# Kernel optimization log

Measured on AMD Instinct MI355X. Metric: run time of the kernel, lower is better.

The kernel has to match this reference:

```python
import jax, jax.numpy as jnp
import numpy as np

H = W = 224
WS = 7          # window size
SS = 3          # shift size
NH = 12         # num heads
N = WS * WS     # tokens per window (49)


def _attn_mask():
    # shift-window attention mask, computed from static ints (numpy)
    img = np.zeros((H, W), np.float32)
    cnt = 0
    for h0, h1 in [(0, H - WS), (H - WS, H - SS), (H - SS, H)]:
        for w0, w1 in [(0, W - WS), (W - WS, W - SS), (W - SS, W)]:
            img[h0:h1, w0:w1] = cnt
            cnt += 1
    mw = img.reshape(H // WS, WS, W // WS, WS).transpose(0, 2, 1, 3).reshape(-1, N)
    diff = mw[:, None, :] - mw[:, :, None]          # (nW, N, N)
    m = np.where(diff != 0, -100.0, 0.0).astype(np.float32)
    return m[:, None, :, :]                         # (nW, 1, N, N)


def _rel_pos_index():
    coords = np.stack(np.meshgrid(np.arange(WS), np.arange(WS), indexing='ij'))
    cf = coords.reshape(2, -1)
    rc = (cf[:, :, None] - cf[:, None, :]).transpose(1, 2, 0)  # (N, N, 2)
    rc[..., 0] += WS - 1
    rc[..., 1] += WS - 1
    rc[..., 0] *= 2 * WS - 1
    return rc.sum(-1).reshape(-1)                    # (N*N,)


_MASK = _attn_mask()
_RPI = _rel_pos_index()


def _ln(x, w, b, eps=1e-5):
    mu = jnp.mean(x, -1, keepdims=True)
    var = jnp.mean((x - mu) ** 2, -1, keepdims=True)
    return (x - mu) / jnp.sqrt(var + eps) * w + b


def setup_inputs() -> dict:
    key = jax.random.key(0)
    ks = jax.random.split(key, 12)
    C, CM = 384, 1536
    s = 0.02
    return {
        'x': jax.random.normal(ks[0], (1, H * W, C), jnp.float32),
        'rpb_table': jax.random.normal(ks[1], (169, NH), jnp.float32) * s,
        'qkv_w': jax.random.normal(ks[2], (3 * C, C), jnp.float32) * s,
        'qkv_b': jax.random.normal(ks[3], (3 * C,), jnp.float32) * s,
        'proj_w': jax.random.normal(ks[4], (C, C), jnp.float32) * s,
        'proj_b': jax.random.normal(ks[5], (C,), jnp.float32) * s,
        'fc1_w': jax.random.normal(ks[6], (CM, C), jnp.float32) * s,
        'fc1_b': jax.random.normal(ks[7], (CM,), jnp.float32) * s,
        'fc2_w': jax.random.normal(ks[8], (C, CM), jnp.float32) * s,
        'fc2_b': jax.random.normal(ks[9], (C,), jnp.float32) * s,
        'norm1_w': jnp.ones((C,), jnp.float32),
        'norm1_b': jnp.zeros((C,), jnp.float32),
        'norm2_w': jnp.ones((C,), jnp.float32),
        'norm2_b': jnp.zeros((C,), jnp.float32),
    }


def reference(x, rpb_table, qkv_w, qkv_b, proj_w, proj_b, fc1_w, fc1_b,
              fc2_w, fc2_b, norm1_w, norm1_b, norm2_w, norm2_b):
    B, L, C = x.shape
    hd = C // NH
    scale = hd ** -0.5
    mask = jnp.asarray(_MASK)                        # (nW, 1, N, N)
    rpi = jnp.asarray(_RPI)

    shortcut = x
    h = _ln(x, norm1_w, norm1_b).reshape(B, H, W, C)
    h = jnp.roll(h, (-SS, -SS), axis=(1, 2))
    # window partition -> (B*nW, N, C)
    win = h.reshape(B, H // WS, WS, W // WS, WS, C).transpose(0, 1, 3, 2, 4, 5)
    win = win.reshape(-1, N, C)

    qkv = (win @ qkv_w.T + qkv_b).reshape(-1, N, 3, NH, hd).transpose(2, 0, 3, 1, 4)
    q, k, v = qkv[0] * scale, qkv[1], qkv[2]         # (nW, NH, N, hd)
    attn = jnp.einsum('whnd,whmd->whnm', q, k)
    bias = rpb_table[rpi].reshape(N, N, NH).transpose(2, 0, 1)[None]  # (1, NH, N, N)
    attn = jax.nn.softmax(attn + bias + mask, axis=-1)
    out = jnp.einsum('whnm,whmd->whnd', attn, v).transpose(0, 2, 1, 3).reshape(-1, N, C)
    out = out @ proj_w.T + proj_b

    # window reverse + unshift
    h = out.reshape(B, H // WS, W // WS, WS, WS, C).transpose(0, 1, 3, 2, 4, 5)
    h = h.reshape(B, H, W, C)
    h = jnp.roll(h, (SS, SS), axis=(1, 2)).reshape(B, L, C)

    x = shortcut + h
    y = _ln(x, norm2_w, norm2_b)
    y = jax.nn.gelu(y @ fc1_w.T + fc1_b, approximate=False)  # torch nn.GELU = erf
    y = y @ fc2_w.T + fc2_b
    return x + y
```

## Files before the change

kernel.cpp:

```cpp
#include <hip/hip_runtime.h>
#include <cstdint>
#include <cstddef>

#define AS1 __attribute__((address_space(1)))
#define AS3 __attribute__((address_space(3)))

typedef __attribute__((ext_vector_type(8))) short bf16x8;
typedef __attribute__((ext_vector_type(4))) short short4v;
typedef __attribute__((ext_vector_type(8))) unsigned short u16x8;
typedef __attribute__((ext_vector_type(4))) float f32x4;
typedef __attribute__((ext_vector_type(4))) unsigned short u16x4;

__device__ __forceinline__ float b2f(uint16_t u){ return __uint_as_float(((uint32_t)u) << 16); }
__device__ __forceinline__ uint16_t f2b(float f){
    uint32_t u = __float_as_uint(f);
    return (uint16_t)((u + 0x7fffu + ((u >> 16) & 1u)) >> 16);
}

__device__ __forceinline__ int pixof(int r){
    int w  = r / 49, t = r - w * 49;
    int wh = w >> 5, ww = w & 31;
    int th = t / 7,  tw = t - th * 7;
    int hp = wh * 7 + th + 3; if (hp >= 224) hp -= 224;
    int wp = ww * 7 + tw + 3; if (wp >= 224) wp -= 224;
    return hp * 224 + wp;
}

__global__ void f2b_kernel(const float* __restrict__ in, uint16_t* __restrict__ out, int n){
    int i = blockIdx.x * 256 + threadIdx.x;
    if (i < n) out[i] = f2b(in[i]);
}

template<int PERM>
__global__ __launch_bounds__(256) void ln_kernel(const float* __restrict__ in,
        const float* __restrict__ g, const float* __restrict__ b, uint16_t* __restrict__ out){
    int wave = threadIdx.x >> 6, lane = threadIdx.x & 63;
    int r = blockIdx.x * 4 + wave;
    int p = PERM ? pixof(r) : r;
    const float* row = in + (size_t)p * 384;
    float a[6];
    #pragma unroll
    for (int i = 0; i < 6; ++i) a[i] = row[lane * 6 + i];
    float s = 0.f, q = 0.f;
    #pragma unroll
    for (int i = 0; i < 6; ++i){ s += a[i]; q += a[i] * a[i]; }
    #pragma unroll
    for (int o = 32; o; o >>= 1){ s += __shfl_xor(s, o); q += __shfl_xor(q, o); }
    float mu   = s * (1.f / 384.f);
    float var  = q * (1.f / 384.f) - mu * mu;
    float rstd = rsqrtf(var + 1e-5f);
    uint16_t* orow = out + (size_t)r * 384;
    #pragma unroll
    for (int i = 0; i < 6; ++i){
        int c = lane * 6 + i;
        orow[c] = f2b((a[i] - mu) * rstd * g[c] + b[c]);
    }
}

template<int EPI>
__global__ __launch_bounds__(256, 2) void gemm_bt(
        const uint16_t* __restrict__ A, const uint16_t* __restrict__ B,
        const float* __restrict__ bias, void* __restrict__ outp,
        const float* __restrict__ xres, int N, int K, int row0)
{
    __shared__ alignas(16) uint16_t lA[128 * 32];
    __shared__ alignas(16) uint16_t lB[128 * 32];
    int tid  = threadIdx.x;
    int lane = tid & 63, wave = tid >> 6;

    int nwg = gridDim.x, bid = blockIdx.x;
    int q8 = nwg >> 3, r8 = nwg & 7;
    int xcd = bid & 7, idx = bid >> 3;
    int wg = (xcd < r8 ? xcd * (q8 + 1) : r8 * (q8 + 1) + (xcd - r8) * q8) + idx;

    int nt = N >> 7;
    int bm = wg / nt, bn = wg - bm * nt;
    int wr = wave >> 1, wc = wave & 1;
    int fr = lane & 15, kc = lane >> 4;

    const uint16_t* Ab = A + (size_t)(bm * 128) * K;
    const uint16_t* Bb = B + (size_t)(bn * 128) * K;
    int row_s = tid >> 2, slot = tid & 3;
    int kchunk = slot ^ (row_s & 3);
    const uint16_t* gA = Ab + (size_t)row_s * K + kchunk * 8;
    const uint16_t* gB = Bb + (size_t)row_s * K + kchunk * 8;
    AS3 char* sA = (AS3 char*)lA;
    AS3 char* sB = (AS3 char*)lB;

    f32x4 acc[4][4] = {};
    for (int k0 = 0; k0 < K; k0 += 32){
        __builtin_amdgcn_global_load_lds((const AS1 void*)(gA + k0),
                                         (AS3 void*)(sA + wave * 1024), 16, 0, 0);
        __builtin_amdgcn_global_load_lds((const AS1 void*)(gA + k0 + (size_t)64 * K),
                                         (AS3 void*)(sA + wave * 1024 + 4096), 16, 0, 0);
        __builtin_amdgcn_global_load_lds((const AS1 void*)(gB + k0),
                                         (AS3 void*)(sB + wave * 1024), 16, 0, 0);
        __builtin_amdgcn_global_load_lds((const AS1 void*)(gB + k0 + (size_t)64 * K),
                                         (AS3 void*)(sB + wave * 1024 + 4096), 16, 0, 0);
        __syncthreads();
        bf16x8 af[4], bv[4];
        #pragma unroll
        for (int m = 0; m < 4; ++m){
            int row = wr * 64 + m * 16 + fr;
            int byt = (row * 64 + kc * 16) ^ ((row & 3) << 4);
            af[m] = *(const bf16x8*)((const char*)lA + byt);
        }
        #pragma unroll
        for (int n = 0; n < 4; ++n){
            int row = wc * 64 + n * 16 + fr;
            int byt = (row * 64 + kc * 16) ^ ((row & 3) << 4);
            bv[n] = *(const bf16x8*)((const char*)lB + byt);
        }
        #pragma unroll
        for (int m = 0; m < 4; ++m)
            #pragma unroll
            for (int n = 0; n < 4; ++n)
                acc[m][n] = __builtin_amdgcn_mfma_f32_16x16x32_bf16(af[m], bv[n], acc[m][n], 0, 0, 0);
        __syncthreads();
    }

    int colb = bn * 128 + wc * 64 + fr;
    int rowb = bm * 128 + wr * 64 + ((lane >> 4) << 2);
    float bvv[4];
    #pragma unroll
    for (int n = 0; n < 4; ++n) bvv[n] = bias[colb + n * 16];

    if constexpr (EPI == 0 || EPI == 1 || EPI == 5){
        uint16_t* out = (uint16_t*)outp;
        #pragma unroll
        for (int m = 0; m < 4; ++m)
            #pragma unroll
            for (int rg = 0; rg < 4; ++rg){
                size_t rr = (size_t)(rowb + m * 16 + rg) * N;
                #pragma unroll
                for (int n = 0; n < 4; ++n){
                    int col = colb + n * 16;
                    float v = acc[m][n][rg] + bvv[n];
                    if constexpr (EPI == 1) v = 0.5f * v * (1.f + erff(v * 0.7071067811865475f));
                    if constexpr (EPI == 5){ if (col < 384) v *= 0.1767766952966369f; }
                    out[rr + col] = f2b(v);
                }
            }
    } else if constexpr (EPI == 2){
        float* out = (float*)outp;
        #pragma unroll
        for (int m = 0; m < 4; ++m)
            #pragma unroll
            for (int rg = 0; rg < 4; ++rg){
                int r = row0 + rowb + m * 16 + rg;
                size_t pb = (size_t)pixof(r) * 384;
                #pragma unroll
                for (int n = 0; n < 4; ++n){
                    int c = colb + n * 16;
                    out[pb + c] = xres[pb + c] + acc[m][n][rg] + bvv[n];
                }
            }
    } else {
        float* out = (float*)outp;
        #pragma unroll
        for (int m = 0; m < 4; ++m)
            #pragma unroll
            for (int rg = 0; rg < 4; ++rg){
                size_t rb2 = (size_t)(rowb + m * 16 + rg) * 384;
                #pragma unroll
                for (int n = 0; n < 4; ++n){
                    int c = colb + n * 16;
                    out[rb2 + c] = out[rb2 + c] + acc[m][n][rg] + bvv[n];
                }
            }
    }
}

__global__ __launch_bounds__(256) void attn_mfma(const uint16_t* __restrict__ qkv,
        const float* __restrict__ rpb, uint16_t* __restrict__ out)
{
    __shared__ float bl[4][208];
    __shared__ uint16_t vtl[4][32][68];
    int wv = threadIdx.x >> 6, lane = threadIdx.x & 63;
    int p = blockIdx.x * 4 + wv;
    int w = p / 12, h = p - w * 12;
    for (int i = lane; i < 169; i += 64) bl[wv][i] = rpb[i * 12 + h];

    const uint16_t* base = qkv + (size_t)(w * 49) * 1152 + h * 32;

    #pragma unroll
    for (int it = 0; it < 4; ++it){
        int u = it * 64 + lane;
        int t = u >> 2, dq = u & 3;
        if (t < 49){
            u16x8 v8 = *(const u16x8*)(base + (size_t)t * 1152 + 768 + dq * 8);
            #pragma unroll
            for (int j = 0; j < 8; ++j) vtl[wv][dq * 8 + j][t] = v8[j];
        } else {
            #pragma unroll
            for (int j = 0; j < 8; ++j) vtl[wv][dq * 8 + j][t] = 0;
        }
    }

    int c = lane & 15, g = lane >> 4;

    bf16x8 qf[4], kf[4];
    #pragma unroll
    for (int nt = 0; nt < 4; ++nt) qf[nt] = *(const bf16x8*)(base + (size_t)(16 * nt + c) * 1152 + g * 8);
    #pragma unroll
    for (int mt = 0; mt < 4; ++mt) kf[mt] = *(const bf16x8*)(base + (size_t)(16 * mt + c) * 1152 + 384 + g * 8);

    f32x4 zero = {0.f, 0.f, 0.f, 0.f};
    f32x4 sv[4][4];
    #pragma unroll
    for (int mt = 0; mt < 4; ++mt)
        #pragma unroll
        for (int nt = 0; nt < 4; ++nt)
            sv[mt][nt] = __builtin_amdgcn_mfma_f32_16x16x32_bf16(kf[mt], qf[nt], zero, 0, 0, 0);

    int wh = w >> 5, ww = w & 31;
    bool edge = (wh == 31) || (ww == 31);
    int ihq[4], iwq[4], regi[4];
    #pragma unroll
    for (int nt = 0; nt < 4; ++nt){
        int q = 16 * nt + c;
        int ih = (q * 37) >> 8; int iw = q - 7 * ih;
        ihq[nt] = ih; iwq[nt] = iw;
        int hi = wh * 7 + ih, wi = ww * 7 + iw;
        regi[nt] = (hi < 217 ? 0 : (hi < 221 ? 1 : 2)) * 3 + (wi < 217 ? 0 : (wi < 221 ? 1 : 2));
    }
    #pragma unroll
    for (int mt = 0; mt < 4; ++mt){
        #pragma unroll
        for (int r = 0; r < 4; ++r){
            int kt = 16 * mt + 4 * g + r;
            int jh = (kt * 37) >> 8; int jw = kt - 7 * jh;
            int hj = wh * 7 + jh, wj = ww * 7 + jw;
            int regj = (hj < 217 ? 0 : (hj < 221 ? 1 : 2)) * 3 + (wj < 217 ? 0 : (wj < 221 ? 1 : 2));
            #pragma unroll
            for (int nt = 0; nt < 4; ++nt){
                float b = bl[wv][(ihq[nt] - jh + 6) * 13 + (iwq[nt] - jw + 6)];
                float add = b + ((edge && regj != regi[nt]) ? -100.f : 0.f);
                float val = sv[mt][nt][r] + add;
                sv[mt][nt][r] = (kt < 49) ? val : -1e9f;
            }
        }
    }

    float inv[4];
    #pragma unroll
    for (int nt = 0; nt < 4; ++nt){
        float mx = -1e30f;
        #pragma unroll
        for (int mt = 0; mt < 4; ++mt)
            #pragma unroll
            for (int r = 0; r < 4; ++r) mx = fmaxf(mx, sv[mt][nt][r]);
        mx = fmaxf(mx, __shfl_xor(mx, 16));
        mx = fmaxf(mx, __shfl_xor(mx, 32));
        float sum = 0.f;
        #pragma unroll
        for (int mt = 0; mt < 4; ++mt)
            #pragma unroll
            for (int r = 0; r < 4; ++r){
                float e = __expf(sv[mt][nt][r] - mx);
                sv[mt][nt][r] = e; sum += e;
            }
        sum += __shfl_xor(sum, 16);
        sum += __shfl_xor(sum, 32);
        inv[nt] = 1.f / sum;
    }

    unsigned pk[4][4][2];
    #pragma unroll
    for (int nt = 0; nt < 4; ++nt)
        #pragma unroll
        for (int mt = 0; mt < 4; ++mt)
            #pragma unroll
            for (int pr = 0; pr < 2; ++pr)
                pk[nt][mt][pr] = (unsigned)f2b(sv[mt][nt][2 * pr]) |
                                 ((unsigned)f2b(sv[mt][nt][2 * pr + 1]) << 16);

    int a0 = (c + 16 * (2 * (g & 1))) * 4;
    int a1 = a0 + 64;
    int sel = g >> 1;

    f32x4 acco[2][4] = {};
    #pragma unroll
    for (int ks = 0; ks < 2; ++ks){
        bf16x8 va[2];
        #pragma unroll
        for (int mt = 0; mt < 2; ++mt){
            short4v lo = *(const short4v*)&vtl[wv][mt * 16 + c][ks * 32 + g * 8];
            short4v hi = *(const short4v*)&vtl[wv][mt * 16 + c][ks * 32 + g * 8 + 4];
            bf16x8 t;
            t[0] = lo[0]; t[1] = lo[1]; t[2] = lo[2]; t[3] = lo[3];
            t[4] = hi[0]; t[5] = hi[1]; t[6] = hi[2]; t[7] = hi[3];
            va[mt] = t;
        }
        #pragma unroll
        for (int nt = 0; nt < 4; ++nt){
            union { unsigned u[4]; bf16x8 v; } pb;
            #pragma unroll
            for (int t = 0; t < 4; ++t){
                int addr = (t >> 1) ? a1 : a0;
                unsigned lo = (unsigned)__builtin_amdgcn_ds_bpermute(addr, (int)pk[nt][2 * ks][t & 1]);
                unsigned hi = (unsigned)__builtin_amdgcn_ds_bpermute(addr, (int)pk[nt][2 * ks + 1][t & 1]);
                pb.u[t] = sel ? hi : lo;
            }
            #pragma unroll
            for (int mt = 0; mt < 2; ++mt)
                acco[mt][nt] = __builtin_amdgcn_mfma_f32_16x16x32_bf16(va[mt], pb.v, acco[mt][nt], 0, 0, 0);
        }
    }

    #pragma unroll
    for (int mt = 0; mt < 2; ++mt)
        #pragma unroll
        for (int nt = 0; nt < 4; ++nt){
            int q = 16 * nt + c;
            if (q < 49){
                u16x4 o;
                #pragma unroll
                for (int r = 0; r < 4; ++r) o[r] = f2b(acco[mt][nt][r] * inv[nt]);
                *(u16x4*)(out + (size_t)(w * 49 + q) * 384 + h * 32 + 16 * mt + 4 * g) = o;
            }
        }
}

extern "C" void kernel_launch(void* const* d_in, const int* in_sizes, int n_in,
                              void* d_out, int out_size, void* d_ws, size_t ws_size,
                              hipStream_t stream) {
    const float* x      = (const float*)d_in[0];
    const float* rpb    = (const float*)d_in[1];
    const float* qkv_w  = (const float*)d_in[2];
    const float* qkv_b  = (const float*)d_in[3];
    const float* proj_w = (const float*)d_in[4];
    const float* proj_b = (const float*)d_in[5];
    const float* fc1_w  = (const float*)d_in[6];
    const float* fc1_b  = (const float*)d_in[7];
    const float* fc2_w  = (const float*)d_in[8];
    const float* fc2_b  = (const float*)d_in[9];
    const float* n1w    = (const float*)d_in[10];
    const float* n1b    = (const float*)d_in[11];
    const float* n2w    = (const float*)d_in[12];
    const float* n2b    = (const float*)d_in[13];

    char* ws = (char*)d_ws;
    uint16_t* winA = (uint16_t*)ws;
    uint16_t* qkB  = (uint16_t*)(ws + 38535168);
    uint16_t* wbuf = (uint16_t*)(ws + 154140672);
    uint16_t* w_qkv  = wbuf;
    uint16_t* w_proj = wbuf + 442368;
    uint16_t* w_fc1  = w_proj + 147456;
    uint16_t* w_fc2  = w_fc1 + 589824;

    f2b_kernel<<<(442368 + 255) / 256, 256, 0, stream>>>(qkv_w, w_qkv, 442368);
    f2b_kernel<<<(147456 + 255) / 256, 256, 0, stream>>>(proj_w, w_proj, 147456);
    f2b_kernel<<<(589824 + 255) / 256, 256, 0, stream>>>(fc1_w, w_fc1, 589824);
    f2b_kernel<<<(589824 + 255) / 256, 256, 0, stream>>>(fc2_w, w_fc2, 589824);

    ln_kernel<1><<<12544, 256, 0, stream>>>(x, n1w, n1b, winA);

    gemm_bt<5><<<392 * 9, 256, 0, stream>>>(winA, w_qkv, qkv_b, qkB, nullptr, 1152, 384, 0);

    attn_mfma<<<3072, 256, 0, stream>>>(qkB, rpb, winA);

    gemm_bt<2><<<392 * 3, 256, 0, stream>>>(winA, w_proj, proj_b, d_out, x, 384, 384, 0);

    ln_kernel<0><<<12544, 256, 0, stream>>>((const float*)d_out, n2w, n2b, winA);

    for (int c2 = 0; c2 < 2; ++c2){
        size_t r0 = (size_t)c2 * 25088;
        gemm_bt<1><<<196 * 12, 256, 0, stream>>>(winA + r0 * 384, w_fc1, fc1_b, qkB, nullptr, 1536, 384, 0);
        gemm_bt<3><<<196 * 3, 256, 0, stream>>>(qkB, w_fc2, fc2_b, (float*)d_out + r0 * 384, nullptr, 384, 1536, 0);
    }
}
```

Before: 431.1 us.

## Double-buffer GEMM LDS tiles and merge weight conversion kernels into one launch

The GEMM main loop now uses two LDS buffers and issues the global-to-LDS loads for the next K tile before computing on the current one. It waits with vmcnt(4) so those loads overlap the MFMA work, where before every iteration stalled on its own load. The four per-weight fp32-to-bf16 conversion launches are also merged into a single launch that picks the source by block index. The cost is twice the LDS per block, which may lower occupancy, plus hand-written waitcnt and barrier ordering that has to stay correct.

```diff
diff --git a/kernel.cpp b/kernel.cpp
--- a/kernel.cpp
+++ b/kernel.cpp
@@ -26,9 +26,18 @@
     return hp * 224 + wp;
 }
 
-__global__ void f2b_kernel(const float* __restrict__ in, uint16_t* __restrict__ out, int n){
-    int i = blockIdx.x * 256 + threadIdx.x;
-    if (i < n) out[i] = f2b(in[i]);
+__global__ void f2b4_kernel(const float* __restrict__ a0, const float* __restrict__ a1,
+                            const float* __restrict__ a2, const float* __restrict__ a3,
+                            uint16_t* __restrict__ o0, uint16_t* __restrict__ o1,
+                            uint16_t* __restrict__ o2, uint16_t* __restrict__ o3){
+    int b = blockIdx.x;
+    const float* src; uint16_t* dst; int base;
+    if (b < 1728)      { src = a0; dst = o0; base = b; }
+    else if (b < 2304) { src = a1; dst = o1; base = b - 1728; }
+    else if (b < 4608) { src = a2; dst = o2; base = b - 2304; }
+    else               { src = a3; dst = o3; base = b - 4608; }
+    int i = base * 256 + threadIdx.x;
+    dst[i] = f2b(src[i]);
 }
 
 template<int PERM>
@@ -63,8 +72,8 @@
         const float* __restrict__ bias, void* __restrict__ outp,
         const float* __restrict__ xres, int N, int K, int row0)
 {
-    __shared__ alignas(16) uint16_t lA[128 * 32];
-    __shared__ alignas(16) uint16_t lB[128 * 32];
+    __shared__ alignas(16) uint16_t lA[2][128 * 32];
+    __shared__ alignas(16) uint16_t lB[2][128 * 32];
     int tid  = threadIdx.x;
     int lane = tid & 63, wave = tid >> 6;
 
@@ -84,39 +93,53 @@
     int kchunk = slot ^ (row_s & 3);
     const uint16_t* gA = Ab + (size_t)row_s * K + kchunk * 8;
     const uint16_t* gB = Bb + (size_t)row_s * K + kchunk * 8;
-    AS3 char* sA = (AS3 char*)lA;
-    AS3 char* sB = (AS3 char*)lB;
+
+    const int NT = K >> 5;
+    auto stage = [&](int t){
+        int buf = t & 1, k0 = t << 5;
+        AS3 char* dA = (AS3 char*)lA[buf] + wave * 1024;
+        AS3 char* dB = (AS3 char*)lB[buf] + wave * 1024;
+        __builtin_amdgcn_global_load_lds((const AS1 void*)(gA + k0), (AS3 void*)dA, 16, 0, 0);
+        __builtin_amdgcn_global_load_lds((const AS1 void*)(gA + k0 + (size_t)64 * K), (AS3 void*)(dA + 4096), 16, 0, 0);
+        __builtin_amdgcn_global_load_lds((const AS1 void*)(gB + k0), (AS3 void*)dB, 16, 0, 0);
+        __builtin_amdgcn_global_load_lds((const AS1 void*)(gB + k0 + (size_t)64 * K), (AS3 void*)(dB + 4096), 16, 0, 0);
+    };
 
     f32x4 acc[4][4] = {};
-    for (int k0 = 0; k0 < K; k0 += 32){
-        __builtin_amdgcn_global_load_lds((const AS1 void*)(gA + k0),
-                                         (AS3 void*)(sA + wave * 1024), 16, 0, 0);
-        __builtin_amdgcn_global_load_lds((const AS1 void*)(gA + k0 + (size_t)64 * K),
-                                         (AS3 void*)(sA + wave * 1024 + 4096), 16, 0, 0);
-        __builtin_amdgcn_global_load_lds((const AS1 void*)(gB + k0),
-                                         (AS3 void*)(sB + wave * 1024), 16, 0, 0);
-        __builtin_amdgcn_global_load_lds((const AS1 void*)(gB + k0 + (size_t)64 * K),
-                                         (AS3 void*)(sB + wave * 1024 + 4096), 16, 0, 0);
-        __syncthreads();
+    stage(0);
+    for (int t = 0; t < NT; ++t){
+        int buf = t & 1;
+        if (t + 1 < NT){
+            stage(t + 1);
+            asm volatile("s_waitcnt vmcnt(4)" ::: "memory");
+        } else {
+            asm volatile("s_waitcnt vmcnt(0)" ::: "memory");
+        }
+        __builtin_amdgcn_s_barrier();
+
         bf16x8 af[4], bv[4];
+        const char* bufA = (const char*)lA[buf];
+        const char* bufB = (const char*)lB[buf];
         #pragma unroll
         for (int m = 0; m < 4; ++m){
             int row = wr * 64 + m * 16 + fr;
             int byt = (row * 64 + kc * 16) ^ ((row & 3) << 4);
-            af[m] = *(const bf16x8*)((const char*)lA + byt);
+            af[m] = *(const bf16x8*)(bufA + byt);
         }
         #pragma unroll
         for (int n = 0; n < 4; ++n){
             int row = wc * 64 + n * 16 + fr;
             int byt = (row * 64 + kc * 16) ^ ((row & 3) << 4);
-            bv[n] = *(const bf16x8*)((const char*)lB + byt);
+            bv[n] = *(const bf16x8*)(bufB + byt);
         }
         #pragma unroll
         for (int m = 0; m < 4; ++m)
             #pragma unroll
             for (int n = 0; n < 4; ++n)
                 acc[m][n] = __builtin_amdgcn_mfma_f32_16x16x32_bf16(af[m], bv[n], acc[m][n], 0, 0, 0);
-        __syncthreads();
+
+        asm volatile("s_waitcnt lgkmcnt(0)" ::: "memory");
+        __builtin_amdgcn_s_barrier();
     }
 
     int colb = bn * 128 + wc * 64 + fr;
@@ -349,10 +372,8 @@
     uint16_t* w_fc1  = w_proj + 147456;
     uint16_t* w_fc2  = w_fc1 + 589824;
 
-    f2b_kernel<<<(442368 + 255) / 256, 256, 0, stream>>>(qkv_w, w_qkv, 442368);
-    f2b_kernel<<<(147456 + 255) / 256, 256, 0, stream>>>(proj_w, w_proj, 147456);
-    f2b_kernel<<<(589824 + 255) / 256, 256, 0, stream>>>(fc1_w, w_fc1, 589824);
-    f2b_kernel<<<(589824 + 255) / 256, 256, 0, stream>>>(fc2_w, w_fc2, 589824);
+    f2b4_kernel<<<6912, 256, 0, stream>>>(qkv_w, proj_w, fc1_w, fc2_w,
+                                          w_qkv, w_proj, w_fc1, w_fc2);
 
     ln_kernel<1><<<12544, 256, 0, stream>>>(x, n1w, n1b, winA);
 
```

Result: slower. 446.9 us (+3.7%).
